# Kernel optimization log

Measured on AMD Instinct MI355X. Metric: run time of the kernel, lower is better.

Reference implementation:

```python
import jax, jax.numpy as jnp
import numpy as np

U = 128  # LSTM units (hardcoded in module)


def _lstm(x_tm, W, Urec, b, return_sequences):
    """Keras-style LSTM. x_tm: [T,B,F] time-major. Gate order i,f,c(g),o.
    activation=tanh, recurrent_activation=sigmoid. recurrent_dropout is
    inference-mode identity (dropout only active in training)."""
    T, B, _ = x_tm.shape
    xz = jnp.einsum('tbf,fg->tbg', x_tm, W) + b  # precompute input projections [T,B,4U]

    def step(carry, xz_t):
        h, c = carry
        z = xz_t + h @ Urec  # [B,4U]
        i, f, g, o = jnp.split(z, 4, axis=-1)
        i = jax.nn.sigmoid(i)
        f = jax.nn.sigmoid(f)
        g = jnp.tanh(g)
        o = jax.nn.sigmoid(o)
        c_new = f * c + i * g
        h_new = o * jnp.tanh(c_new)
        return (h_new, c_new), h_new

    h0 = jnp.zeros((B, U), x_tm.dtype)
    c0 = jnp.zeros((B, U), x_tm.dtype)
    (h_last, _), hs = jax.lax.scan(step, (h0, c0), xz)
    return hs if return_sequences else h_last


def setup_inputs() -> dict:
    key = jax.random.key(0)
    ks = jax.random.split(key, 7)
    B, T, F = 512, 256, 64
    s_in = 1.0 / np.sqrt(F)
    s_rec = 1.0 / np.sqrt(U)
    return {
        'x': jax.random.normal(ks[0], (B, T, F), jnp.float32),
        'W1': jax.random.normal(ks[1], (F, 4 * U), jnp.float32) * s_in,
        'U1': jax.random.normal(ks[2], (U, 4 * U), jnp.float32) * s_rec,
        'b1': jnp.zeros((4 * U,), jnp.float32),
        'W2': jax.random.normal(ks[3], (U, 4 * U), jnp.float32) * s_rec,
        'U2': jax.random.normal(ks[4], (U, 4 * U), jnp.float32) * s_rec,
        'b2': jnp.zeros((4 * U,), jnp.float32),
        'Wd': jax.random.normal(ks[5], (U, 1), jnp.float32) * s_rec,
        'bd': jnp.zeros((1,), jnp.float32),
    }


def reference(x, W1, U1, b1, W2, U2, b2, Wd, bd):
    x_tm = jnp.transpose(x, (1, 0, 2))  # [T,B,F]
    hs = _lstm(x_tm, W1, U1, b1, return_sequences=True)   # hidden_lstm -> [T,B,U]
    h_last = _lstm(hs, W2, U2, b2, return_sequences=False)  # lstm_layer -> [B,U]
    return jax.nn.relu(h_last @ Wd + bd)  # Dense(1, relu) -> [B,1]
```

## Files before the change

### kernel.cpp

```cpp
#include <hip/hip_runtime.h>


#define T_STEPS 256
#define BATCH   512
#define NU      128
#define FDIM    64

typedef _Float16 h8 __attribute__((ext_vector_type(8)));
typedef _Float16 h4 __attribute__((ext_vector_type(4)));
typedef float    f4 __attribute__((ext_vector_type(4)));

#define LOG2E    1.4426950408889634f
#define TWOLOG2E 2.8853900817779268f

#define WG_BARRIER() asm volatile("s_waitcnt lgkmcnt(0)\n\ts_barrier" ::: "memory")

#if __has_builtin(__builtin_amdgcn_exp2f)
#define EXP2F(x) __builtin_amdgcn_exp2f(x)
#else
#define EXP2F(x) exp2f(x)
#endif
#if __has_builtin(__builtin_amdgcn_rcpf)
#define RCPF(x) __builtin_amdgcn_rcpf(x)
#else
#define RCPF(x) (1.0f / (x))
#endif

__device__ __forceinline__ float sigm2(float s) {
    return RCPF(1.0f + EXP2F(s));
}
__device__ __forceinline__ float tanh2(float t) {
    return 1.0f - 2.0f * RCPF(1.0f + EXP2F(t));
}

__global__ void prep_weights(const float* __restrict__ W1, const float* __restrict__ U1,
                             const float* __restrict__ b1, const float* __restrict__ W2,
                             const float* __restrict__ U2, const float* __restrict__ b2,
                             _Float16* __restrict__ Wp1, _Float16* __restrict__ Up1,
                             _Float16* __restrict__ Wp2, _Float16* __restrict__ Up2,
                             float* __restrict__ bp1, float* __restrict__ bp2) {
    int i = blockIdx.x * 256 + threadIdx.x;
    if (i < 32768) {
        int col = i >> 6, k = i & 63;
        float sc = ((col >> 7) == 2) ? TWOLOG2E : -LOG2E;
        Wp1[i] = (_Float16)(W1[k * 512 + col] * sc);
    } else if (i < 32768 + 65536) {
        int j = i - 32768; int col = j >> 7, k = j & 127;
        float sc = ((col >> 7) == 2) ? TWOLOG2E : -LOG2E;
        Up1[j] = (_Float16)(U1[k * 512 + col] * sc);
    } else if (i < 32768 + 131072) {
        int j = i - 98304; int col = j >> 7, k = j & 127;
        float sc = ((col >> 7) == 2) ? TWOLOG2E : -LOG2E;
        Wp2[j] = (_Float16)(W2[k * 512 + col] * sc);
    } else if (i < 32768 + 196608) {
        int j = i - 163840; int col = j >> 7, k = j & 127;
        float sc = ((col >> 7) == 2) ? TWOLOG2E : -LOG2E;
        Up2[j] = (_Float16)(U2[k * 512 + col] * sc);
    } else if (i < 32768 + 196608 + 1024) {
        int j = i - 229376;
        if (j < 512) {
            float sc = ((j >> 7) == 2) ? TWOLOG2E : -LOG2E;
            bp1[j] = b1[j] * sc;
        } else {
            int col = j - 512;
            float sc = ((col >> 7) == 2) ? TWOLOG2E : -LOG2E;
            bp2[col] = b2[col] * sc;
        }
    }
}

template <bool IS_A>
__attribute__((amdgpu_waves_per_eu(2, 2)))
__global__ __launch_bounds__(512) void lstm_layer(
    const float* __restrict__ xA, const _Float16* __restrict__ xB,
    const _Float16* __restrict__ Wp,
    const _Float16* __restrict__ Up,
    const float* __restrict__ bp,
    _Float16* __restrict__ hs_out,
    const float* __restrict__ Wd, const float* __restrict__ bd,
    float* __restrict__ dout) {
    constexpr int KX  = IS_A ? 64 : 128;
    constexpr int KXS = KX / 32;
    constexpr int PH  = 136;
    constexpr int H0  = 0;
    constexpr int H1  = 2 * PH;

    __shared__ __align__(16) _Float16 smh[4 * PH];
    __shared__ __align__(16) float smxz[2 * 8192];

    const int tid  = threadIdx.x;
    const int lane = tid & 63;
    const int wv   = tid >> 6;
    const int m    = lane & 15;
    const int kc   = lane >> 4;
    const int u0   = wv * 16;
    const int b0   = blockIdx.x * 2;

    for (int i = tid; i < 4 * PH; i += 512) smh[i] = (_Float16)0.0f;

    h8 uf[4][4];
#pragma unroll
    for (int g = 0; g < 4; g++)
#pragma unroll
        for (int ks = 0; ks < 4; ks++)
            uf[g][ks] = *(const h8*)&Up[(g * 128 + u0 + m) * 128 + ks * 32 + kc * 8];
    h8 wf[4][KXS];
#pragma unroll
    for (int g = 0; g < 4; g++)
#pragma unroll
        for (int ks = 0; ks < KXS; ks++)
            wf[g][ks] = *(const h8*)&Wp[(g * 128 + u0 + m) * KX + ks * 32 + kc * 8];
    float bias[4];
#pragma unroll
    for (int g = 0; g < 4; g++) bias[g] = bp[g * 128 + u0 + m];

    f4 rX[4]; h8 rH[4];
    auto loadA = [&](int kblk) {
        int tt = kblk * 8 + (m >> 1); if (tt > T_STEPS - 1) tt = T_STEPS - 1;
        const int bb = b0 + (m & 1);
        if constexpr (IS_A) {
#pragma unroll
            for (int ks = 0; ks < KXS; ks++)
#pragma unroll
                for (int hf = 0; hf < 2; hf++)
                    rX[ks * 2 + hf] = *(const f4*)&xA[((size_t)bb * T_STEPS + tt) * FDIM
                                                      + ks * 32 + kc * 8 + hf * 4];
        } else {
#pragma unroll
            for (int ks = 0; ks < 4; ks++)
                rH[ks] = *(const h8*)&xB[((size_t)tt * BATCH + bb) * NU + ks * 32 + kc * 8];
        }
    };
    auto calcX = [&](int kblk) {
        float* xzw = &smxz[(kblk & 1) * 8192];
        f4 accx[4];
#pragma unroll
        for (int g = 0; g < 4; g++) accx[g] = (f4){bias[g], bias[g], bias[g], bias[g]};
#pragma unroll
        for (int ks = 0; ks < KXS; ks++) {
            h8 a;
            if constexpr (IS_A) {
#pragma unroll
                for (int j = 0; j < 4; j++) {
                    a[j]     = (_Float16)rX[ks * 2][j];
                    a[4 + j] = (_Float16)rX[ks * 2 + 1][j];
                }
            } else {
                a = rH[ks];
            }
#pragma unroll
            for (int g = 0; g < 4; g++)
                accx[g] = __builtin_amdgcn_mfma_f32_16x16x32_f16(a, wf[g][ks], accx[g], 0, 0, 0);
        }
#pragma unroll
        for (int rr = 0; rr < 4; rr++) {
            f4 v = {accx[0][rr], accx[1][rr], accx[2][rr], accx[3][rr]};
            *(f4*)&xzw[((kc * 4 + rr) * 128 + u0 + m) * 4] = v;
        }
    };

    loadA(0); calcX(0);
    loadA(1);
    __syncthreads();

    const h8 hzero = {};
    h8 ha[4];
#pragma unroll
    for (int ks = 0; ks < 4; ks++) ha[ks] = hzero;

    f4 fzero = (f4){0.f, 0.f, 0.f, 0.f};
    asm volatile("" : "+v"(fzero));

    const int erow = lane >> 4;
    float cst = 0.0f;

#pragma unroll 16
    for (int t = 0; t < T_STEPS; t++) {
        const int p = t & 1;
        const int s = t & 7;
        const int half = (t >> 3) & 1;

        if (s == 0) {
            int kn = (t >> 3) + 1;
            if (kn < T_STEPS / 8) {
                calcX(kn);
                loadA(kn + 1);
            }
        }

        f4 xzv;
        if (lane < 32)
            xzv = *(const f4*)&smxz[half * 8192 + (s * 2 + erow) * 512 + (u0 + m) * 4];

        if (m == 0 || m == 4) {
            const _Float16* hb = &smh[(p ? H1 : H0) + (m == 4 ? PH : 0)];
#pragma unroll
            for (int ks = 0; ks < 4; ks++)
                ha[ks] = *(const h8*)&hb[ks * 32 + kc * 8];
        }

        f4 acc[4];
#pragma unroll
        for (int g = 0; g < 4; g++)
            acc[g] = __builtin_amdgcn_mfma_f32_16x16x32_f16(ha[0], uf[g][0], fzero, 0, 0, 0);
#pragma unroll
        for (int ks = 1; ks < 4; ks++)
#pragma unroll
            for (int g = 0; g < 4; g++)
                acc[g] = __builtin_amdgcn_mfma_f32_16x16x32_f16(ha[ks], uf[g][ks], acc[g], 0, 0, 0);

        if (lane < 32) {
            float gi = sigm2(acc[0][0] + xzv[0]);
            float gf = sigm2(acc[1][0] + xzv[1]);
            float gg = tanh2(acc[2][0] + xzv[2]);
            float go = sigm2(acc[3][0] + xzv[3]);
            cst = gf * cst + gi * gg;
            float hv = go * tanh2(cst * TWOLOG2E);
            _Float16 h16 = (_Float16)hv;
            smh[(p ? H0 : H1) + erow * PH + u0 + m] = h16;
            if constexpr (IS_A)
                hs_out[((size_t)t * BATCH + b0 + erow) * NU + u0 + m] = h16;
        }
        WG_BARRIER();
    }

    if constexpr (!IS_A) {
        if (wv == 0) {
            int rw = lane >> 5, u = lane & 31;
            float sacc = 0.0f;
#pragma unroll
            for (int j = 0; j < 4; j++) {
                int uum = u + j * 32;
                sacc += (float)smh[H0 + rw * PH + uum] * Wd[uum];
            }
            sacc += __shfl_xor(sacc, 16);
            sacc += __shfl_xor(sacc, 8);
            sacc += __shfl_xor(sacc, 4);
            sacc += __shfl_xor(sacc, 2);
            sacc += __shfl_xor(sacc, 1);
            if ((lane & 31) == 0) dout[b0 + rw] = fmaxf(sacc + bd[0], 0.0f);
        }
    }
}

extern "C" void kernel_launch(void* const* d_in, const int* in_sizes, int n_in,
                              void* d_out, int out_size, void* d_ws, size_t ws_size,
                              hipStream_t stream) {
    const float* x  = (const float*)d_in[0];
    const float* W1 = (const float*)d_in[1];
    const float* U1 = (const float*)d_in[2];
    const float* b1 = (const float*)d_in[3];
    const float* W2 = (const float*)d_in[4];
    const float* U2 = (const float*)d_in[5];
    const float* b2 = (const float*)d_in[6];
    const float* Wd = (const float*)d_in[7];
    const float* bd = (const float*)d_in[8];
    float* out = (float*)d_out;

    const size_t HS   = 33554432;
    const size_t oWp1 = HS;
    const size_t oUp1 = oWp1 + 65536;
    const size_t oWp2 = oUp1 + 131072;
    const size_t oUp2 = oWp2 + 131072;
    const size_t oBp1 = oUp2 + 131072;
    const size_t oBp2 = oBp1 + 2048;
    const size_t need = oBp2 + 2048;
    if (ws_size < need) return;

    char* ws = (char*)d_ws;
    _Float16* hs  = (_Float16*)ws;
    _Float16* Wp1 = (_Float16*)(ws + oWp1);
    _Float16* Up1 = (_Float16*)(ws + oUp1);
    _Float16* Wp2 = (_Float16*)(ws + oWp2);
    _Float16* Up2 = (_Float16*)(ws + oUp2);
    float*    bp1 = (float*)(ws + oBp1);
    float*    bp2 = (float*)(ws + oBp2);

    prep_weights<<<900, 256, 0, stream>>>(W1, U1, b1, W2, U2, b2,
                                          Wp1, Up1, Wp2, Up2, bp1, bp2);
    lstm_layer<true><<<256, 512, 0, stream>>>(x, nullptr, Wp1, Up1, bp1,
                                              hs, nullptr, nullptr, nullptr);
    lstm_layer<false><<<256, 512, 0, stream>>>(nullptr, hs, Wp2, Up2, bp2,
                                               nullptr, Wd, bd, out);
}
```

Measured before the change: 352.1 us.

## Fuse both LSTM layers into one skewed wavefront kernel with LDS ring buffer

Runs both LSTM layers in a single kernel, with layer 2 lagging layer 1 by 16 timesteps. Layer 1's hidden states go into an LDS ring buffer and are consumed by layer 2's input projection, so the global hs write/read round trip and the second launch are gone. Lanes 0-31 compute layer-1 gates and lanes 32-63 compute layer-2 gates in the same wave, so the two serial recurrences share each per-step barrier. The cost is more registers (both recurrent weight sets kept resident), input weights now reloaded from global memory in every projection call, and more MFMA work per step, which could lengthen the critical path.

```diff
diff --git a/kernel.cpp b/kernel.cpp
--- a/kernel.cpp
+++ b/kernel.cpp
@@ -5,9 +5,10 @@
 #define BATCH   512
 #define NU      128
 #define FDIM    64
+#define SKEW    16
+#define NITER   (T_STEPS + SKEW)
 
 typedef _Float16 h8 __attribute__((ext_vector_type(8)));
-typedef _Float16 h4 __attribute__((ext_vector_type(4)));
 typedef float    f4 __attribute__((ext_vector_type(4)));
 
 #define LOG2E    1.4426950408889634f
@@ -69,24 +70,22 @@
     }
 }
 
-template <bool IS_A>
+#define XROW  516
+#define XHALF (16 * XROW)
+#define PH    136
+
 __attribute__((amdgpu_waves_per_eu(2, 2)))
-__global__ __launch_bounds__(512) void lstm_layer(
-    const float* __restrict__ xA, const _Float16* __restrict__ xB,
-    const _Float16* __restrict__ Wp,
-    const _Float16* __restrict__ Up,
-    const float* __restrict__ bp,
-    _Float16* __restrict__ hs_out,
+__global__ __launch_bounds__(512) void lstm_fused(
+    const float* __restrict__ xA,
+    const _Float16* __restrict__ Wp1, const _Float16* __restrict__ Up1,
+    const _Float16* __restrict__ Wp2, const _Float16* __restrict__ Up2,
+    const float* __restrict__ bp1, const float* __restrict__ bp2,
     const float* __restrict__ Wd, const float* __restrict__ bd,
     float* __restrict__ dout) {
-    constexpr int KX  = IS_A ? 64 : 128;
-    constexpr int KXS = KX / 32;
-    constexpr int PH  = 136;
-    constexpr int H0  = 0;
-    constexpr int H1  = 2 * PH;
-
-    __shared__ __align__(16) _Float16 smh[4 * PH];
-    __shared__ __align__(16) float smxz[2 * 8192];
+    __shared__ __align__(16) float smxzA[2 * XHALF];
+    __shared__ __align__(16) float smxzB[2 * XHALF];
+    __shared__ __align__(16) _Float16 ringA[32 * PH];
+    __shared__ __align__(16) _Float16 ringB[4 * PH];
 
     const int tid  = threadIdx.x;
     const int lane = tid & 63;
@@ -95,151 +94,194 @@
     const int kc   = lane >> 4;
     const int u0   = wv * 16;
     const int b0   = blockIdx.x * 2;
-
-    for (int i = tid; i < 4 * PH; i += 512) smh[i] = (_Float16)0.0f;
-
-    h8 uf[4][4];
+    const bool isB = lane >= 32;
+    const int erow = (lane >> 4) & 1;
+
+    for (int i = tid; i < 32 * PH; i += 512) ringA[i] = (_Float16)0.0f;
+    for (int i = tid; i < 4 * PH; i += 512) ringB[i] = (_Float16)0.0f;
+
+    h8 uf1[4][4], uf2[4][4];
 #pragma unroll
     for (int g = 0; g < 4; g++)
 #pragma unroll
-        for (int ks = 0; ks < 4; ks++)
-            uf[g][ks] = *(const h8*)&Up[(g * 128 + u0 + m) * 128 + ks * 32 + kc * 8];
-    h8 wf[4][KXS];
-#pragma unroll
-    for (int g = 0; g < 4; g++)
-#pragma unroll
-        for (int ks = 0; ks < KXS; ks++)
-            wf[g][ks] = *(const h8*)&Wp[(g * 128 + u0 + m) * KX + ks * 32 + kc * 8];
-    float bias[4];
-#pragma unroll
-    for (int g = 0; g < 4; g++) bias[g] = bp[g * 128 + u0 + m];
-
-    f4 rX[4]; h8 rH[4];
+        for (int ks = 0; ks < 4; ks++) {
+            uf1[g][ks] = *(const h8*)&Up1[(g * 128 + u0 + m) * 128 + ks * 32 + kc * 8];
+            uf2[g][ks] = *(const h8*)&Up2[(g * 128 + u0 + m) * 128 + ks * 32 + kc * 8];
+        }
+    float biasA[4], biasB[4];
+#pragma unroll
+    for (int g = 0; g < 4; g++) {
+        biasA[g] = bp1[g * 128 + u0 + m];
+        biasB[g] = bp2[g * 128 + u0 + m];
+    }
+
+    f4 rX[4];
     auto loadA = [&](int kblk) {
         int tt = kblk * 8 + (m >> 1); if (tt > T_STEPS - 1) tt = T_STEPS - 1;
         const int bb = b0 + (m & 1);
-        if constexpr (IS_A) {
-#pragma unroll
-            for (int ks = 0; ks < KXS; ks++)
-#pragma unroll
-                for (int hf = 0; hf < 2; hf++)
-                    rX[ks * 2 + hf] = *(const f4*)&xA[((size_t)bb * T_STEPS + tt) * FDIM
-                                                      + ks * 32 + kc * 8 + hf * 4];
-        } else {
-#pragma unroll
-            for (int ks = 0; ks < 4; ks++)
-                rH[ks] = *(const h8*)&xB[((size_t)tt * BATCH + bb) * NU + ks * 32 + kc * 8];
-        }
+#pragma unroll
+        for (int ks = 0; ks < 2; ks++)
+#pragma unroll
+            for (int hf = 0; hf < 2; hf++)
+                rX[ks * 2 + hf] = *(const f4*)&xA[((size_t)bb * T_STEPS + tt) * FDIM
+                                                  + ks * 32 + kc * 8 + hf * 4];
     };
-    auto calcX = [&](int kblk) {
-        float* xzw = &smxz[(kblk & 1) * 8192];
+    auto calcXA = [&](int kblk) {
+        float* xzw = &smxzA[(kblk & 1) * XHALF];
         f4 accx[4];
 #pragma unroll
-        for (int g = 0; g < 4; g++) accx[g] = (f4){bias[g], bias[g], bias[g], bias[g]};
-#pragma unroll
-        for (int ks = 0; ks < KXS; ks++) {
+        for (int g = 0; g < 4; g++) accx[g] = (f4){biasA[g], biasA[g], biasA[g], biasA[g]};
+#pragma unroll
+        for (int ks = 0; ks < 2; ks++) {
             h8 a;
-            if constexpr (IS_A) {
-#pragma unroll
-                for (int j = 0; j < 4; j++) {
-                    a[j]     = (_Float16)rX[ks * 2][j];
-                    a[4 + j] = (_Float16)rX[ks * 2 + 1][j];
-                }
-            } else {
-                a = rH[ks];
+#pragma unroll
+            for (int j = 0; j < 4; j++) {
+                a[j]     = (_Float16)rX[ks * 2][j];
+                a[4 + j] = (_Float16)rX[ks * 2 + 1][j];
             }
-#pragma unroll
-            for (int g = 0; g < 4; g++)
-                accx[g] = __builtin_amdgcn_mfma_f32_16x16x32_f16(a, wf[g][ks], accx[g], 0, 0, 0);
+            h8 w[4];
+#pragma unroll
+            for (int g = 0; g < 4; g++)
+                w[g] = *(const h8*)&Wp1[(g * 128 + u0 + m) * 64 + ks * 32 + kc * 8];
+#pragma unroll
+            for (int g = 0; g < 4; g++)
+                accx[g] = __builtin_amdgcn_mfma_f32_16x16x32_f16(a, w[g], accx[g], 0, 0, 0);
         }
 #pragma unroll
         for (int rr = 0; rr < 4; rr++) {
             f4 v = {accx[0][rr], accx[1][rr], accx[2][rr], accx[3][rr]};
-            *(f4*)&xzw[((kc * 4 + rr) * 128 + u0 + m) * 4] = v;
+            *(f4*)&xzw[(kc * 4 + rr) * XROW + (u0 + m) * 4] = v;
         }
     };
-
-    loadA(0); calcX(0);
+    auto calcXB = [&](int jb) {
+        float* xzw = &smxzB[(jb & 1) * XHALF];
+        const _Float16* rb = &ringA[((jb & 1) * 16 + (m >> 1) * 2 + (m & 1)) * PH];
+        f4 accx[4];
+#pragma unroll
+        for (int g = 0; g < 4; g++) accx[g] = (f4){biasB[g], biasB[g], biasB[g], biasB[g]};
+#pragma unroll
+        for (int ks = 0; ks < 4; ks++) {
+            h8 a = *(const h8*)&rb[ks * 32 + kc * 8];
+            h8 w[4];
+#pragma unroll
+            for (int g = 0; g < 4; g++)
+                w[g] = *(const h8*)&Wp2[(g * 128 + u0 + m) * 128 + ks * 32 + kc * 8];
+#pragma unroll
+            for (int g = 0; g < 4; g++)
+                accx[g] = __builtin_amdgcn_mfma_f32_16x16x32_f16(a, w[g], accx[g], 0, 0, 0);
+        }
+#pragma unroll
+        for (int rr = 0; rr < 4; rr++) {
+            f4 v = {accx[0][rr], accx[1][rr], accx[2][rr], accx[3][rr]};
+            *(f4*)&xzw[(kc * 4 + rr) * XROW + (u0 + m) * 4] = v;
+        }
+    };
+
+    loadA(0); calcXA(0);
     loadA(1);
     __syncthreads();
 
     const h8 hzero = {};
-    h8 ha[4];
-#pragma unroll
-    for (int ks = 0; ks < 4; ks++) ha[ks] = hzero;
+    h8 ha[4], hb[4];
+#pragma unroll
+    for (int ks = 0; ks < 4; ks++) { ha[ks] = hzero; hb[ks] = hzero; }
 
     f4 fzero = (f4){0.f, 0.f, 0.f, 0.f};
     asm volatile("" : "+v"(fzero));
 
-    const int erow = lane >> 4;
     float cst = 0.0f;
 
 #pragma unroll 16
-    for (int t = 0; t < T_STEPS; t++) {
-        const int p = t & 1;
-        const int s = t & 7;
-        const int half = (t >> 3) & 1;
-
-        if (s == 0) {
-            int kn = (t >> 3) + 1;
+    for (int i = 0; i < NITER; i++) {
+        const int tB = i - SKEW;
+
+        if ((i & 7) == 0) {
+            int kn = (i >> 3) + 1;
             if (kn < T_STEPS / 8) {
-                calcX(kn);
+                calcXA(kn);
                 loadA(kn + 1);
             }
+            int jb = (i >> 3) - 1;
+            if (jb >= 0 && jb < T_STEPS / 8) calcXB(jb);
         }
 
         f4 xzv;
-        if (lane < 32)
-            xzv = *(const f4*)&smxz[half * 8192 + (s * 2 + erow) * 512 + (u0 + m) * 4];
-
-        if (m == 0 || m == 4) {
-            const _Float16* hb = &smh[(p ? H1 : H0) + (m == 4 ? PH : 0)];
-#pragma unroll
-            for (int ks = 0; ks < 4; ks++)
-                ha[ks] = *(const h8*)&hb[ks * 32 + kc * 8];
-        }
-
-        f4 acc[4];
-#pragma unroll
-        for (int g = 0; g < 4; g++)
-            acc[g] = __builtin_amdgcn_mfma_f32_16x16x32_f16(ha[0], uf[g][0], fzero, 0, 0, 0);
-#pragma unroll
-        for (int ks = 1; ks < 4; ks++)
-#pragma unroll
-            for (int g = 0; g < 4; g++)
-                acc[g] = __builtin_amdgcn_mfma_f32_16x16x32_f16(ha[ks], uf[g][ks], acc[g], 0, 0, 0);
-
-        if (lane < 32) {
-            float gi = sigm2(acc[0][0] + xzv[0]);
-            float gf = sigm2(acc[1][0] + xzv[1]);
-            float gg = tanh2(acc[2][0] + xzv[2]);
-            float go = sigm2(acc[3][0] + xzv[3]);
+        {
+            const float* pa = &smxzA[((i  >> 3) & 1) * XHALF + ((i  & 7) * 2 + erow) * XROW + (u0 + m) * 4];
+            const float* pb = &smxzB[((tB >> 3) & 1) * XHALF + ((tB & 7) * 2 + erow) * XROW + (u0 + m) * 4];
+            xzv = *(const f4*)(isB ? pb : pa);
+        }
+
+        if ((m & 3) == 0) {
+            const int br = (m >> 2) & 1;
+            const _Float16* hp = (m & 8)
+                ? &ringB[((tB & 1) * 2 + br) * PH]
+                : &ringA[(((i - 1) & 15) * 2 + br) * PH];
+            h8 f0 = *(const h8*)&hp[0 * 32 + kc * 8];
+            h8 f1 = *(const h8*)&hp[1 * 32 + kc * 8];
+            h8 f2 = *(const h8*)&hp[2 * 32 + kc * 8];
+            h8 f3 = *(const h8*)&hp[3 * 32 + kc * 8];
+            if (m & 8) { hb[0] = f0; hb[1] = f1; hb[2] = f2; hb[3] = f3; }
+            else       { ha[0] = f0; ha[1] = f1; ha[2] = f2; ha[3] = f3; }
+        }
+
+        f4 accA[4], accB[4];
+        if (i < T_STEPS) {
+#pragma unroll
+            for (int g = 0; g < 4; g++)
+                accA[g] = __builtin_amdgcn_mfma_f32_16x16x32_f16(ha[0], uf1[g][0], fzero, 0, 0, 0);
+#pragma unroll
+            for (int ks = 1; ks < 4; ks++)
+#pragma unroll
+                for (int g = 0; g < 4; g++)
+                    accA[g] = __builtin_amdgcn_mfma_f32_16x16x32_f16(ha[ks], uf1[g][ks], accA[g], 0, 0, 0);
+        }
+        if (tB >= 0) {
+#pragma unroll
+            for (int g = 0; g < 4; g++)
+                accB[g] = __builtin_amdgcn_mfma_f32_16x16x32_f16(hb[0], uf2[g][0], fzero, 0, 0, 0);
+#pragma unroll
+            for (int ks = 1; ks < 4; ks++)
+#pragma unroll
+                for (int g = 0; g < 4; g++)
+                    accB[g] = __builtin_amdgcn_mfma_f32_16x16x32_f16(hb[ks], uf2[g][ks], accB[g], 0, 0, 0);
+        }
+
+        const bool act = isB ? (tB >= 0) : (i < T_STEPS);
+        if (act) {
+            float zi = (isB ? accB[0][0] : accA[0][0]) + xzv[0];
+            float zf = (isB ? accB[1][0] : accA[1][0]) + xzv[1];
+            float zg = (isB ? accB[2][0] : accA[2][0]) + xzv[2];
+            float zo = (isB ? accB[3][0] : accA[3][0]) + xzv[3];
+            float gi = sigm2(zi);
+            float gf = sigm2(zf);
+            float gg = tanh2(zg);
+            float go = sigm2(zo);
             cst = gf * cst + gi * gg;
             float hv = go * tanh2(cst * TWOLOG2E);
             _Float16 h16 = (_Float16)hv;
-            smh[(p ? H0 : H1) + erow * PH + u0 + m] = h16;
-            if constexpr (IS_A)
-                hs_out[((size_t)t * BATCH + b0 + erow) * NU + u0 + m] = h16;
+            _Float16* wp = isB
+                ? &ringB[(((tB & 1) ^ 1) * 2 + erow) * PH + u0 + m]
+                : &ringA[((i & 15) * 2 + erow) * PH + u0 + m];
+            *wp = h16;
         }
         WG_BARRIER();
     }
 
-    if constexpr (!IS_A) {
-        if (wv == 0) {
-            int rw = lane >> 5, u = lane & 31;
-            float sacc = 0.0f;
-#pragma unroll
-            for (int j = 0; j < 4; j++) {
-                int uum = u + j * 32;
-                sacc += (float)smh[H0 + rw * PH + uum] * Wd[uum];
-            }
-            sacc += __shfl_xor(sacc, 16);
-            sacc += __shfl_xor(sacc, 8);
-            sacc += __shfl_xor(sacc, 4);
-            sacc += __shfl_xor(sacc, 2);
-            sacc += __shfl_xor(sacc, 1);
-            if ((lane & 31) == 0) dout[b0 + rw] = fmaxf(sacc + bd[0], 0.0f);
-        }
+    if (wv == 0) {
+        int rw = lane >> 5, u = lane & 31;
+        float sacc = 0.0f;
+#pragma unroll
+        for (int j = 0; j < 4; j++) {
+            int uu = u + j * 32;
+            sacc += (float)ringB[rw * PH + uu] * Wd[uu];
+        }
+        sacc += __shfl_xor(sacc, 16);
+        sacc += __shfl_xor(sacc, 8);
+        sacc += __shfl_xor(sacc, 4);
+        sacc += __shfl_xor(sacc, 2);
+        sacc += __shfl_xor(sacc, 1);
+        if ((lane & 31) == 0) dout[b0 + rw] = fmaxf(sacc + bd[0], 0.0f);
     }
 }
 
@@ -257,8 +299,7 @@
     const float* bd = (const float*)d_in[8];
     float* out = (float*)d_out;
 
-    const size_t HS   = 33554432;
-    const size_t oWp1 = HS;
+    const size_t oWp1 = 0;
     const size_t oUp1 = oWp1 + 65536;
     const size_t oWp2 = oUp1 + 131072;
     const size_t oUp2 = oWp2 + 131072;
@@ -268,7 +309,6 @@
     if (ws_size < need) return;
 
     char* ws = (char*)d_ws;
-    _Float16* hs  = (_Float16*)ws;
     _Float16* Wp1 = (_Float16*)(ws + oWp1);
     _Float16* Up1 = (_Float16*)(ws + oUp1);
     _Float16* Wp2 = (_Float16*)(ws + oWp2);
@@ -278,8 +318,6 @@
 
     prep_weights<<<900, 256, 0, stream>>>(W1, U1, b1, W2, U2, b2,
                                           Wp1, Up1, Wp2, Up2, bp1, bp2);
-    lstm_layer<true><<<256, 512, 0, stream>>>(x, nullptr, Wp1, Up1, bp1,
-                                              hs, nullptr, nullptr, nullptr);
-    lstm_layer<false><<<256, 512, 0, stream>>>(nullptr, hs, Wp2, Up2, bp2,
-                                               nullptr, Wd, bd, out);
-}
+    lstm_fused<<<256, 512, 0, stream>>>(x, Wp1, Up1, Wp2, Up2, bp1, bp2,
+                                        Wd, bd, out);
+}
```

Result: slower. 795.8 us (+126.0%).

## Process 16 batch rows per block with fused input projection and swizzled LDS

Applied to the files above, without the earlier changes.

Each LSTM workgroup now handles 16 batch rows instead of 2, so the MFMA M dimension is fully used and only 32 blocks launch per layer. The per-block precomputed xz buffer in LDS is dropped. Instead the input projection is computed inside every timestep as extra MFMAs accumulated with the recurrent product, while the next step's inputs are prefetched from global memory. Weights are pinned in AGPRs through inline asm MFMA, and the LDS hidden state uses an XOR swizzle to avoid bank conflicts. The trade is far fewer CUs in use (32 of the GPU's CUs) and more serial per-step work in exchange for better MFMA utilisation and less duplicated weight loading.

```diff
diff --git a/kernel.cpp b/kernel.cpp
--- a/kernel.cpp
+++ b/kernel.cpp
@@ -7,13 +7,19 @@
 #define FDIM    64
 
 typedef _Float16 h8 __attribute__((ext_vector_type(8)));
-typedef _Float16 h4 __attribute__((ext_vector_type(4)));
 typedef float    f4 __attribute__((ext_vector_type(4)));
 
 #define LOG2E    1.4426950408889634f
 #define TWOLOG2E 2.8853900817779268f
 
 #define WG_BARRIER() asm volatile("s_waitcnt lgkmcnt(0)\n\ts_barrier" ::: "memory")
+
+#define MFMA16(d, a, b, c) \
+    asm("v_mfma_f32_16x16x32_f16 %0, %1, %2, %3" : "=&v"(d) : "v"(a), "a"(b), "v"(c))
+#define MFMA16_ACC(d, a, b) \
+    asm("v_mfma_f32_16x16x32_f16 %0, %1, %2, %0" : "+v"(d) : "v"(a), "a"(b))
+#define MFMA16_END(d, a, b) \
+    asm("v_mfma_f32_16x16x32_f16 %0, %1, %2, %0\n\ts_nop 7" : "+v"(d) : "v"(a), "a"(b))
 
 #if __has_builtin(__builtin_amdgcn_exp2f)
 #define EXP2F(x) __builtin_amdgcn_exp2f(x)
@@ -69,176 +75,171 @@
     }
 }
 
+__device__ __forceinline__ int hidx(int row, int k) {
+    return row * 128 + ((((k >> 3) ^ (row & 7)) << 3) | (k & 7));
+}
+
 template <bool IS_A>
-__attribute__((amdgpu_waves_per_eu(2, 2)))
-__global__ __launch_bounds__(512) void lstm_layer(
-    const float* __restrict__ xA, const _Float16* __restrict__ xB,
+__global__ __launch_bounds__(512)
+__attribute__((amdgpu_waves_per_eu(2, 2))) void lstm16(
+    const float* __restrict__ xA, const _Float16* __restrict__ hsIn,
     const _Float16* __restrict__ Wp,
     const _Float16* __restrict__ Up,
     const float* __restrict__ bp,
-    _Float16* __restrict__ hs_out,
+    _Float16* __restrict__ hsOut,
     const float* __restrict__ Wd, const float* __restrict__ bd,
     float* __restrict__ dout) {
-    constexpr int KX  = IS_A ? 64 : 128;
-    constexpr int KXS = KX / 32;
-    constexpr int PH  = 136;
-    constexpr int H0  = 0;
-    constexpr int H1  = 2 * PH;
-
-    __shared__ __align__(16) _Float16 smh[4 * PH];
-    __shared__ __align__(16) float smxz[2 * 8192];
+    constexpr int KH = IS_A ? 2 : 4;
+
+    __shared__ __align__(16) _Float16 smh[4096];
 
     const int tid  = threadIdx.x;
     const int lane = tid & 63;
     const int wv   = tid >> 6;
-    const int m    = lane & 15;
-    const int kc   = lane >> 4;
+    const int r15  = lane & 15;
+    const int q    = lane >> 4;
     const int u0   = wv * 16;
-    const int b0   = blockIdx.x * 2;
-
-    for (int i = tid; i < 4 * PH; i += 512) smh[i] = (_Float16)0.0f;
-
-    h8 uf[4][4];
-#pragma unroll
-    for (int g = 0; g < 4; g++)
-#pragma unroll
-        for (int ks = 0; ks < 4; ks++)
-            uf[g][ks] = *(const h8*)&Up[(g * 128 + u0 + m) * 128 + ks * 32 + kc * 8];
-    h8 wf[4][KXS];
-#pragma unroll
-    for (int g = 0; g < 4; g++)
-#pragma unroll
-        for (int ks = 0; ks < KXS; ks++)
-            wf[g][ks] = *(const h8*)&Wp[(g * 128 + u0 + m) * KX + ks * 32 + kc * 8];
+    const int row0 = blockIdx.x * 16;
+
+    for (int i = tid; i < 4096; i += 512) smh[i] = (_Float16)0.0f;
+
+    h8 uf[4][4], wf[4][KH];
+#pragma unroll
+    for (int g = 0; g < 4; g++) {
+#pragma unroll
+        for (int ks = 0; ks < 4; ks++) {
+            uf[g][ks] = *(const h8*)&Up[(g * 128 + u0 + r15) * 128 + ks * 32 + q * 8];
+            asm("" : "+a"(uf[g][ks]));
+        }
+#pragma unroll
+        for (int ks = 0; ks < KH; ks++) {
+            wf[g][ks] = *(const h8*)&Wp[(g * 128 + u0 + r15) * (KH * 32) + ks * 32 + q * 8];
+            asm("" : "+a"(wf[g][ks]));
+        }
+    }
     float bias[4];
 #pragma unroll
-    for (int g = 0; g < 4; g++) bias[g] = bp[g * 128 + u0 + m];
-
-    f4 rX[4]; h8 rH[4];
-    auto loadA = [&](int kblk) {
-        int tt = kblk * 8 + (m >> 1); if (tt > T_STEPS - 1) tt = T_STEPS - 1;
-        const int bb = b0 + (m & 1);
-        if constexpr (IS_A) {
-#pragma unroll
-            for (int ks = 0; ks < KXS; ks++)
-#pragma unroll
-                for (int hf = 0; hf < 2; hf++)
-                    rX[ks * 2 + hf] = *(const f4*)&xA[((size_t)bb * T_STEPS + tt) * FDIM
-                                                      + ks * 32 + kc * 8 + hf * 4];
-        } else {
-#pragma unroll
-            for (int ks = 0; ks < 4; ks++)
-                rH[ks] = *(const h8*)&xB[((size_t)tt * BATCH + bb) * NU + ks * 32 + kc * 8];
-        }
-    };
-    auto calcX = [&](int kblk) {
-        float* xzw = &smxz[(kblk & 1) * 8192];
-        f4 accx[4];
-#pragma unroll
-        for (int g = 0; g < 4; g++) accx[g] = (f4){bias[g], bias[g], bias[g], bias[g]};
-#pragma unroll
-        for (int ks = 0; ks < KXS; ks++) {
-            h8 a;
-            if constexpr (IS_A) {
-#pragma unroll
-                for (int j = 0; j < 4; j++) {
-                    a[j]     = (_Float16)rX[ks * 2][j];
-                    a[4 + j] = (_Float16)rX[ks * 2 + 1][j];
-                }
-            } else {
-                a = rH[ks];
-            }
-#pragma unroll
-            for (int g = 0; g < 4; g++)
-                accx[g] = __builtin_amdgcn_mfma_f32_16x16x32_f16(a, wf[g][ks], accx[g], 0, 0, 0);
-        }
-#pragma unroll
-        for (int rr = 0; rr < 4; rr++) {
-            f4 v = {accx[0][rr], accx[1][rr], accx[2][rr], accx[3][rr]};
-            *(f4*)&xzw[((kc * 4 + rr) * 128 + u0 + m) * 4] = v;
-        }
-    };
-
-    loadA(0); calcX(0);
-    loadA(1);
-    __syncthreads();
-
-    const h8 hzero = {};
-    h8 ha[4];
-#pragma unroll
-    for (int ks = 0; ks < 4; ks++) ha[ks] = hzero;
+    for (int g = 0; g < 4; g++) bias[g] = bp[g * 128 + u0 + r15];
+
+    f4 cst = {0.0f, 0.0f, 0.0f, 0.0f};
 
     f4 fzero = (f4){0.f, 0.f, 0.f, 0.f};
     asm volatile("" : "+v"(fzero));
 
-    const int erow = lane >> 4;
-    float cst = 0.0f;
-
-#pragma unroll 16
-    for (int t = 0; t < T_STEPS; t++) {
-        const int p = t & 1;
-        const int s = t & 7;
-        const int half = (t >> 3) & 1;
-
-        if (s == 0) {
-            int kn = (t >> 3) + 1;
-            if (kn < T_STEPS / 8) {
-                calcX(kn);
-                loadA(kn + 1);
-            }
-        }
-
-        f4 xzv;
-        if (lane < 32)
-            xzv = *(const f4*)&smxz[half * 8192 + (s * 2 + erow) * 512 + (u0 + m) * 4];
-
-        if (m == 0 || m == 4) {
-            const _Float16* hb = &smh[(p ? H1 : H0) + (m == 4 ? PH : 0)];
+    h8 xa[2][KH];
+    f4 xraw[4];
+
+    auto loadFragB = [&](h8* dst, int t) {
+        if constexpr (!IS_A) {
+            const _Float16* p = &hsIn[((size_t)t * BATCH + row0 + r15) * NU + q * 8];
 #pragma unroll
             for (int ks = 0; ks < 4; ks++)
-                ha[ks] = *(const h8*)&hb[ks * 32 + kc * 8];
-        }
-
-        f4 acc[4];
-#pragma unroll
-        for (int g = 0; g < 4; g++)
-            acc[g] = __builtin_amdgcn_mfma_f32_16x16x32_f16(ha[0], uf[g][0], fzero, 0, 0, 0);
-#pragma unroll
-        for (int ks = 1; ks < 4; ks++)
+                dst[ks] = *(const h8*)(p + ks * 32);
+        }
+    };
+    auto loadXraw = [&](int t) {
+        if constexpr (IS_A) {
+            const float* p = &xA[((size_t)(row0 + r15) * T_STEPS + t) * FDIM + q * 8];
+#pragma unroll
+            for (int ks = 0; ks < 2; ks++) {
+                xraw[ks * 2]     = *(const f4*)(p + ks * 32);
+                xraw[ks * 2 + 1] = *(const f4*)(p + ks * 32 + 4);
+            }
+        }
+    };
+
+    if constexpr (IS_A) loadXraw(0);
+    else                loadFragB(xa[0], 0);
+    __syncthreads();
+
+    for (int k = 0; k < 32; k++) {
+#pragma unroll
+        for (int s = 0; s < 8; s++) {
+            const int t = k * 8 + s;
+            const int tn = (t + 1 > 255) ? 255 : t + 1;
+
+            h8 xc[2];
+            if constexpr (IS_A) {
+#pragma unroll
+                for (int ks = 0; ks < 2; ks++) {
+                    h8 a;
+#pragma unroll
+                    for (int j = 0; j < 4; j++) {
+                        a[j]     = (_Float16)xraw[ks * 2][j];
+                        a[4 + j] = (_Float16)xraw[ks * 2 + 1][j];
+                    }
+                    xc[ks] = a;
+                }
+                loadXraw(tn);
+            } else {
+                loadFragB(xa[(s & 1) ^ 1], tn);
+            }
+
+            h8 ha[4];
+            {
+                const int rb = (((s & 1) ^ 1) << 11) + r15 * 128;
+#pragma unroll
+                for (int ks = 0; ks < 4; ks++)
+                    ha[ks] = *(const h8*)&smh[rb + (((ks * 4 + q) ^ (r15 & 7)) << 3)];
+            }
+
+            f4 az[4];
+            if constexpr (IS_A) {
+#pragma unroll
+                for (int g = 0; g < 4; g++)
+                    MFMA16(az[g], xc[0], wf[g][0], fzero);
+#pragma unroll
+                for (int g = 0; g < 4; g++)
+                    MFMA16_ACC(az[g], xc[1], wf[g][1]);
+            } else {
+#pragma unroll
+                for (int g = 0; g < 4; g++)
+                    MFMA16(az[g], xa[s & 1][0], wf[g][0], fzero);
+#pragma unroll
+                for (int ks = 1; ks < 4; ks++)
+#pragma unroll
+                    for (int g = 0; g < 4; g++)
+                        MFMA16_ACC(az[g], xa[s & 1][ks], wf[g][ks]);
+            }
+#pragma unroll
+            for (int ks = 0; ks < 3; ks++)
+#pragma unroll
+                for (int g = 0; g < 4; g++)
+                    MFMA16_ACC(az[g], ha[ks], uf[g][ks]);
 #pragma unroll
             for (int g = 0; g < 4; g++)
-                acc[g] = __builtin_amdgcn_mfma_f32_16x16x32_f16(ha[ks], uf[g][ks], acc[g], 0, 0, 0);
-
-        if (lane < 32) {
-            float gi = sigm2(acc[0][0] + xzv[0]);
-            float gf = sigm2(acc[1][0] + xzv[1]);
-            float gg = tanh2(acc[2][0] + xzv[2]);
-            float go = sigm2(acc[3][0] + xzv[3]);
-            cst = gf * cst + gi * gg;
-            float hv = go * tanh2(cst * TWOLOG2E);
-            _Float16 h16 = (_Float16)hv;
-            smh[(p ? H0 : H1) + erow * PH + u0 + m] = h16;
-            if constexpr (IS_A)
-                hs_out[((size_t)t * BATCH + b0 + erow) * NU + u0 + m] = h16;
-        }
-        WG_BARRIER();
+                MFMA16_END(az[g], ha[3], uf[g][3]);
+
+#pragma unroll
+            for (int rr = 0; rr < 4; rr++) {
+                float gi = sigm2(az[0][rr] + bias[0]);
+                float gf = sigm2(az[1][rr] + bias[1]);
+                float gg = tanh2(az[2][rr] + bias[2]);
+                float go = sigm2(az[3][rr] + bias[3]);
+                cst[rr] = gf * cst[rr] + gi * gg;
+                float hv = go * tanh2(cst[rr] * TWOLOG2E);
+                _Float16 h16 = (_Float16)hv;
+                const int rowp = q * 4 + rr;
+                smh[((s & 1) << 11) + hidx(rowp, u0 + r15)] = h16;
+                if constexpr (IS_A)
+                    hsOut[((size_t)t * BATCH + row0 + rowp) * NU + u0 + r15] = h16;
+            }
+            WG_BARRIER();
+        }
     }
 
     if constexpr (!IS_A) {
         if (wv == 0) {
-            int rw = lane >> 5, u = lane & 31;
+            const int row = lane >> 2, kk = lane & 3;
             float sacc = 0.0f;
 #pragma unroll
-            for (int j = 0; j < 4; j++) {
-                int uum = u + j * 32;
-                sacc += (float)smh[H0 + rw * PH + uum] * Wd[uum];
-            }
-            sacc += __shfl_xor(sacc, 16);
-            sacc += __shfl_xor(sacc, 8);
-            sacc += __shfl_xor(sacc, 4);
+            for (int j = 0; j < 32; j++) {
+                int kx = kk + 4 * j;
+                sacc += (float)smh[2048 + hidx(row, kx)] * Wd[kx];
+            }
             sacc += __shfl_xor(sacc, 2);
             sacc += __shfl_xor(sacc, 1);
-            if ((lane & 31) == 0) dout[b0 + rw] = fmaxf(sacc + bd[0], 0.0f);
+            if (kk == 0) dout[row0 + row] = fmaxf(sacc + bd[0], 0.0f);
         }
     }
 }
@@ -278,8 +279,8 @@
 
     prep_weights<<<900, 256, 0, stream>>>(W1, U1, b1, W2, U2, b2,
                                           Wp1, Up1, Wp2, Up2, bp1, bp2);
-    lstm_layer<true><<<256, 512, 0, stream>>>(x, nullptr, Wp1, Up1, bp1,
-                                              hs, nullptr, nullptr, nullptr);
-    lstm_layer<false><<<256, 512, 0, stream>>>(nullptr, hs, Wp2, Up2, bp2,
-                                               nullptr, Wd, bd, out);
-}
+    lstm16<true><<<32, 512, 0, stream>>>(x, nullptr, Wp1, Up1, bp1,
+                                         hs, nullptr, nullptr, nullptr);
+    lstm16<false><<<32, 512, 0, stream>>>(nullptr, hs, Wp2, Up2, bp2,
+                                          nullptr, Wd, bd, out);
+}
```

Measured after the change: 699.1 us. +98.6%, slower.
